# Optimization experiments

Measured on AMD Instinct MI355X. Metric: run time of the kernel, lower is better.

## Reference

```python
import jax, jax.numpy as jnp
import numpy as np
from jax.scipy.linalg import expm

N, D, COND_DIM = 1152, 64, 1152
B, T = 16, 1024


def setup_inputs() -> dict:
    key = jax.random.key(0)
    k1, k2, k3, k4, k5 = jax.random.split(key, 5)
    x = jax.random.normal(k1, (B, T, N), dtype=jnp.float32)
    cond = jax.random.normal(k2, (B, COND_DIM), dtype=jnp.float32)
    # learned parameters
    P = jax.random.normal(k3, (N, D), dtype=jnp.float32)
    n_skew = D * (D - 1) // 2
    # nn.Linear default init: U(-1/sqrt(fan_in), 1/sqrt(fan_in))
    bound = 1.0 / np.sqrt(COND_DIM)
    W = jax.random.uniform(k4, (n_skew, COND_DIM), minval=-bound, maxval=bound, dtype=jnp.float32)
    b = jax.random.uniform(k5, (n_skew,), minval=-bound, maxval=bound, dtype=jnp.float32)
    return {"x": x, "cond": cond, "P": P, "W": W, "b": b}


def _rotation(cond, W, b):
    # SiLU -> Linear -> skew-symmetric A -> matrix exponential
    v = jax.nn.silu(cond) @ W.T + b  # (B, D*(D-1)//2)
    iu, ju = jnp.triu_indices(D, k=1)
    A = jnp.zeros((cond.shape[0], D, D), dtype=v.dtype)
    A = A.at[:, iu, ju].set(v).at[:, ju, iu].set(-v)
    return expm(A)  # batched over leading dim, (B, D, D)


def reference(x, cond, P, W, b):
    U, _ = jnp.linalg.qr(P)          # (N, D) orthonormal basis of subspace
    R = _rotation(cond, W, b)        # (B, D, D)
    z = jnp.einsum('btn,nd->btd', x, U)          # project into subspace
    z_rot = jnp.einsum('btd,bde->bte', z, R)     # rotate within subspace
    x_rot = x + jnp.einsum('btd,nd->btn', z_rot - z, U)  # (z_rot - z) @ U.T
    return x_rot
```

## Files before the change

### kernel.cpp

```cpp
#include <hip/hip_runtime.h>
#include <math.h>

#define NN 1152
#define DD 64
#define NSK 2016
#define NB 16
#define NROWS (NB*1024)
#define GPARTS 6
#define KPARTS 6
#define VNBLK 32
#define VBLKS (VNBLK*KPARTS)
#define TOFF (VBLKS + GPARTS)
#define TBLKS 18

typedef short bf16x8 __attribute__((ext_vector_type(8)));
typedef short bf16x4 __attribute__((ext_vector_type(4)));
typedef float f32x4  __attribute__((ext_vector_type(4)));

__device__ __forceinline__ short bfr(float f){
  unsigned u = __float_as_uint(f);
  u += 0x7fffu + ((u >> 16) & 1u);
  return (short)(u >> 16);
}
__device__ __forceinline__ float htof(short h){
  return __uint_as_float(((unsigned)(unsigned short)h) << 16);
}

__global__ __launch_bounds__(256) void k_pre(const float* __restrict__ cond, const float* __restrict__ W,
                                             float* __restrict__ vpart,
                                             const float* __restrict__ P, float* __restrict__ Gpart,
                                             short* __restrict__ Pbf, short* __restrict__ Ptbf){
  __shared__ float Ps[64*68];
  const int tid = threadIdx.x;
  if (blockIdx.x < VBLKS){
    const int nb = blockIdx.x / KPARTS;
    const int kp = blockIdx.x % KPARTS;
    const int lane = tid & 63, wid = tid >> 6;
    const int m = lane & 15, quad = lane >> 4;
    const int n0 = nb*64 + wid*16;
    if (n0 >= NSK) return;
    f32x4 acc = {0.f,0.f,0.f,0.f};
    const float* crow = &cond[m*NN + kp*192 + quad*8];
    const float* wrow = &W[(n0 + m)*NN + kp*192 + quad*8];
    #pragma unroll
    for (int c = 0; c < 6; ++c){
      const float4 ca = *(const float4*)(crow + c*32);
      const float4 cb = *(const float4*)(crow + c*32 + 4);
      const float4 wa = *(const float4*)(wrow + c*32);
      const float4 wb = *(const float4*)(wrow + c*32 + 4);
      bf16x8 a, b;
      const float cv[8] = {ca.x,ca.y,ca.z,ca.w,cb.x,cb.y,cb.z,cb.w};
      const float wv[8] = {wa.x,wa.y,wa.z,wa.w,wb.x,wb.y,wb.z,wb.w};
      #pragma unroll
      for (int j = 0; j < 8; ++j){
        const float xv = cv[j];
        a[j] = bfr(xv / (1.f + __expf(-xv)));
        b[j] = bfr(wv[j]);
      }
      acc = __builtin_amdgcn_mfma_f32_16x16x32_bf16(a, b, acc, 0, 0, 0);
    }
    #pragma unroll
    for (int r = 0; r < 4; ++r)
      vpart[(kp*16 + quad*4 + r)*NSK + n0 + m] = acc[r];
  } else if (blockIdx.x < TOFF){
    const int p = blockIdx.x - VBLKS;
    const int lr = tid >> 4, lc = (tid & 15) * 4;
    const int ti = tid >> 4, tj = tid & 15;
    float acc[4][4];
    #pragma unroll
    for (int i=0;i<4;++i){
      #pragma unroll
      for (int j=0;j<4;++j) acc[i][j]=0.f;
    }
    for (int ch = 0; ch < 3; ++ch){
      const int nn0 = p*192 + ch*64;
      __syncthreads();
      #pragma unroll
      for (int ii = 0; ii < 4; ++ii){
        const float4 pv = *(const float4*)&P[(nn0 + lr + 16*ii)*DD + lc];
        *(float4*)&Ps[(lr + 16*ii)*68 + lc] = pv;
      }
      __syncthreads();
      for (int r = 0; r < 64; ++r){
        const float4 a = *(const float4*)&Ps[r*68 + ti*4];
        const float4 b = *(const float4*)&Ps[r*68 + tj*4];
        const float av[4] = {a.x,a.y,a.z,a.w};
        const float bv[4] = {b.x,b.y,b.z,b.w};
        #pragma unroll
        for (int i=0;i<4;++i){
          #pragma unroll
          for (int j=0;j<4;++j) acc[i][j] = fmaf(av[i], bv[j], acc[i][j]);
        }
      }
    }
    float* g = &Gpart[p*DD*DD];
    #pragma unroll
    for (int i=0;i<4;++i){
      float4 ov = make_float4(acc[i][0], acc[i][1], acc[i][2], acc[i][3]);
      *(float4*)&g[(ti*4+i)*DD + tj*4] = ov;
    }
  } else {
    const int t = blockIdx.x - TOFF;
    const int n0 = t*64;
    for (int idx = tid; idx < 4096; idx += 256)
      Ps[(idx>>6)*68 + (idx&63)] = P[(n0 + (idx>>6))*DD + (idx&63)];
    __syncthreads();
    for (int idx = tid; idx < 4096; idx += 256){
      const int r = idx>>6, c = idx&63;
      Pbf[(n0+r)*DD + c] = bfr(Ps[r*68 + c]);
    }
    for (int idx = tid; idx < 4096; idx += 256){
      const int d = idx>>6, rr = idx&63;
      Ptbf[d*NN + n0 + rr] = bfr(Ps[rr*68 + d]);
    }
  }
}

__device__ __forceinline__ void mmul68(const float* __restrict__ A, const float* __restrict__ B,
                                       float* __restrict__ C, int tid){
  __syncthreads();
  const int w = tid >> 6, lane = tid & 63;
  const int r0 = (w & 3) * 16 + (lane >> 3) * 2;
  const int c0 = (w >> 2) * 32 + (lane & 7) * 4;
  float acc[2][4];
  #pragma unroll
  for (int i=0;i<2;++i){
    #pragma unroll
    for (int j=0;j<4;++j) acc[i][j]=0.f;
  }
  float4 b0 = *(const float4*)&B[0*68 + c0];
  float4 b1 = *(const float4*)&B[1*68 + c0];
  float4 b2 = *(const float4*)&B[2*68 + c0];
  float4 b3 = *(const float4*)&B[3*68 + c0];
  float4 a0 = *(const float4*)&A[(r0    )*68];
  float4 a1 = *(const float4*)&A[(r0 + 1)*68];
  for (int kq = 0; kq < 16; ++kq){
    float4 nb0, nb1, nb2, nb3, na0, na1;
    if (kq < 15){
      const int k4 = (kq+1)*4;
      nb0 = *(const float4*)&B[(k4+0)*68 + c0];
      nb1 = *(const float4*)&B[(k4+1)*68 + c0];
      nb2 = *(const float4*)&B[(k4+2)*68 + c0];
      nb3 = *(const float4*)&B[(k4+3)*68 + c0];
      na0 = *(const float4*)&A[(r0    )*68 + k4];
      na1 = *(const float4*)&A[(r0 + 1)*68 + k4];
    }
    const float av0[4] = {a0.x,a0.y,a0.z,a0.w};
    const float av1[4] = {a1.x,a1.y,a1.z,a1.w};
    const float4 bb[4] = {b0,b1,b2,b3};
    #pragma unroll
    for (int kk=0;kk<4;++kk){
      acc[0][0] = fmaf(av0[kk], bb[kk].x, acc[0][0]);
      acc[0][1] = fmaf(av0[kk], bb[kk].y, acc[0][1]);
      acc[0][2] = fmaf(av0[kk], bb[kk].z, acc[0][2]);
      acc[0][3] = fmaf(av0[kk], bb[kk].w, acc[0][3]);
      acc[1][0] = fmaf(av1[kk], bb[kk].x, acc[1][0]);
      acc[1][1] = fmaf(av1[kk], bb[kk].y, acc[1][1]);
      acc[1][2] = fmaf(av1[kk], bb[kk].z, acc[1][2]);
      acc[1][3] = fmaf(av1[kk], bb[kk].w, acc[1][3]);
    }
    b0 = nb0; b1 = nb1; b2 = nb2; b3 = nb3; a0 = na0; a1 = na1;
  }
  *(float4*)&C[(r0    )*68 + c0] = make_float4(acc[0][0],acc[0][1],acc[0][2],acc[0][3]);
  *(float4*)&C[(r0 + 1)*68 + c0] = make_float4(acc[1][0],acc[1][1],acc[1][2],acc[1][3]);
  __syncthreads();
}

__global__ __launch_bounds__(512,1) void k_fused(const float* __restrict__ Gpart, const float* __restrict__ P,
                                                 const float* __restrict__ vpart, const float* __restrict__ bias,
                                                 float* __restrict__ Mg, float* __restrict__ Rg,
                                                 const float* __restrict__ x, const short* __restrict__ Ptbf,
                                                 short* __restrict__ ybf){
  __shared__ float Bs[64*68], B2[64*68], B3[64*68], Tb[64*68], Xb[64*68];
  __shared__ float red[512];
  __shared__ float scl_s;
  __shared__ int   ssh_s;
  const int tid = threadIdx.x;
  if (blockIdx.x > NB){
    const int lane = tid & 63, wid = tid >> 6;
    const int row0 = (blockIdx.x - NB - 1) * 64;
    const int m    = lane & 15, quad = lane >> 4;
    const int r0 = (wid & 3) * 16;
    const int c0 = (wid >> 2) * 32;
    f32x4 acc0 = {0.f,0.f,0.f,0.f}, acc1 = {0.f,0.f,0.f,0.f};
    const float* xrow = &x[(row0 + r0 + m)*NN + quad*8];
    const short* ut0  = &Ptbf[(c0      + m)*NN + quad*8];
    const short* ut1  = &Ptbf[(c0 + 16 + m)*NN + quad*8];
    float4 xa = *(const float4*)(xrow);
    float4 xb = *(const float4*)(xrow + 4);
    bf16x8 b0 = *(const bf16x8*)(ut0);
    bf16x8 b1 = *(const bf16x8*)(ut1);
    for (int kc = 0; kc < NN; kc += 32){
      float4 nxa, nxb; bf16x8 nb0, nb1;
      if (kc + 32 < NN){
        nxa = *(const float4*)(xrow + kc + 32);
        nxb = *(const float4*)(xrow + kc + 36);
        nb0 = *(const bf16x8*)(ut0 + kc + 32);
        nb1 = *(const bf16x8*)(ut1 + kc + 32);
      }
      bf16x8 a;
      a[0]=bfr(xa.x); a[1]=bfr(xa.y); a[2]=bfr(xa.z); a[3]=bfr(xa.w);
      a[4]=bfr(xb.x); a[5]=bfr(xb.y); a[6]=bfr(xb.z); a[7]=bfr(xb.w);
      acc0 = __builtin_amdgcn_mfma_f32_16x16x32_bf16(a, b0, acc0, 0, 0, 0);
      acc1 = __builtin_amdgcn_mfma_f32_16x16x32_bf16(a, b1, acc1, 0, 0, 0);
      xa = nxa; xb = nxb; b0 = nb0; b1 = nb1;
    }
    #pragma unroll
    for (int q = 0; q < 4; ++q){
      ybf[(row0 + r0 + quad*4 + q)*DD + c0      + m] = bfr(acc0[q]);
      ybf[(row0 + r0 + quad*4 + q)*DD + c0 + 16 + m] = bfr(acc1[q]);
    }
    return;
  }
  if (blockIdx.x == NB){
    if (tid < 64){
      const int j = tid;
      float Gc[DD], Wc[DD], Rc[DD];
      #pragma unroll
      for (int i = 0; i < DD; ++i){
        float g = 0.f;
        #pragma unroll
        for (int p = 0; p < GPARTS; ++p) g += Gpart[p*4096 + i*DD + j];
        Gc[i] = g;
        Wc[i] = P[i*DD + j];
      }
      #pragma unroll
      for (int k = 0; k < DD; ++k){
        const float gkk = __shfl(Gc[k], k);
        const float wkk = __shfl(Wc[k], k);
        const float beta = (wkk >= 0.f) ? -sqrtf(gkk) : sqrtf(gkk);
        const float wkj = Wc[k];
        const float dj  = Gc[k] - beta*wkj;
        const float cj  = dj / (beta*(beta - wkk));
        float rkj = wkj + dj/beta;
        if (j == k) rkj = beta;
        if (j <  k) rkj = 0.f;
        Rc[k] = rkj;
        #pragma unroll
        for (int i = k+1; i < DD; ++i){
          const float wik = __shfl(Wc[i], k);
          const float rki = __shfl(rkj, i);
          Wc[i] = fmaf(-cj,  wik, Wc[i]);
          Gc[i] = fmaf(-rki, rkj, Gc[i]);
        }
      }
      #pragma unroll
      for (int i = 0; i < DD; ++i) Rg[i*DD + j] = Rc[i];
    }
    return;
  }
  const int b = blockIdx.x;
  for (int idx = tid; idx < 64*64; idx += 512)
    Xb[(idx>>6)*68 + (idx&63)] = 0.f;
  __syncthreads();
  for (int idx = tid; idx < NSK; idx += 512){
    int i = (int)((127.0f - sqrtf(16129.0f - 8.0f*(float)idx)) * 0.5f);
    while (i*(127 - i)/2 > idx) --i;
    while ((i+1)*(127 - (i+1))/2 <= idx) ++i;
    const int jj = idx - i*(127 - i)/2 + i + 1;
    float val = bias[idx];
    #pragma unroll
    for (int p = 0; p < KPARTS; ++p) val += vpart[(p*16 + b)*NSK + idx];
    Xb[i*68 + jj] = val;
    Xb[jj*68 + i] = -val;
  }
  __syncthreads();
  {
    const int c = tid & 63, g = tid >> 6;
    float s = 0.f;
    for (int r = g*8; r < g*8 + 8; ++r) s += fabsf(Xb[r*68 + c]);
    red[g*64 + c] = s;
    __syncthreads();
    if (tid < 64){
      float cs = 0.f;
      #pragma unroll
      for (int g2 = 0; g2 < 8; ++g2) cs += red[g2*64 + tid];
      #pragma unroll
      for (int off = 32; off > 0; off >>= 1) cs = fmaxf(cs, __shfl_xor(cs, off));
      if (tid == 0){
        int s2 = 0; float scale = 1.f;
        float nrm = cs;
        while (nrm > 1.0f && s2 < 40){ nrm *= 0.5f; scale *= 0.5f; ++s2; }
        ssh_s = s2; scl_s = scale;
      }
    }
    __syncthreads();
  }
  const float scale = scl_s;
  const int   sq    = ssh_s;
  for (int idx = tid; idx < 64*64; idx += 512){
    const int i = idx>>6, jj = idx&63;
    Bs[i*68 + jj] = Xb[i*68 + jj] * scale;
  }
  mmul68(Bs, Bs, B2, tid);
  mmul68(B2, Bs, B3, tid);
  for (int idx = tid; idx < 64*64; idx += 512){
    const int i = idx>>6, jj = idx&63;
    const int o = i*68 + jj;
    Tb[o] = (i==jj ? (1.f/720.f) : 0.f) + Bs[o]*(1.f/5040.f) + B2[o]*(1.f/40320.f) + B3[o]*(1.f/362880.f);
  }
  mmul68(B3, Tb, Xb, tid);
  for (int idx = tid; idx < 64*64; idx += 512){
    const int i = idx>>6, jj = idx&63;
    const int o = i*68 + jj;
    Xb[o] += (i==jj ? (1.f/6.f) : 0.f) + Bs[o]*(1.f/24.f) + B2[o]*(1.f/120.f);
  }
  mmul68(B3, Xb, Tb, tid);
  for (int idx = tid; idx < 64*64; idx += 512){
    const int i = idx>>6, jj = idx&63;
    const int o = i*68 + jj;
    Tb[o] += (i==jj ? 1.f : 0.f) + Bs[o] + B2[o]*0.5f;
  }
  float* cur = Tb;
  float* oth = Xb;
  for (int r = 0; r < sq; ++r){
    mmul68(cur, cur, oth, tid);
    float* t = cur; cur = oth; oth = t;
  }
  for (int idx = tid; idx < 64*64; idx += 512){
    const int i = idx>>6, jj = idx&63;
    Mg[b*4096 + idx] = cur[i*68 + jj] - (i==jj ? 1.f : 0.f);
  }
}

__global__ __launch_bounds__(256) void k_kmat(const float* __restrict__ Rg, const float* __restrict__ Mg,
                                              float* __restrict__ Kg){
  __shared__ float Ri[64*68], Ms[64*68], Ts[64*68];
  __shared__ float rd[64];
  const int b = blockIdx.x, tid = threadIdx.x;
  float* Rf = Ts;
  for (int idx = tid; idx < 4096; idx += 256){
    Rf[idx] = Rg[idx];
    Ms[(idx>>6)*68 + (idx&63)] = Mg[b*4096 + idx];
  }
  __syncthreads();
  if (tid < 64) rd[tid] = 1.f / Rf[tid*DD + tid];
  __syncthreads();
  if (tid < 64){
    float u[DD];
    #pragma unroll
    for (int j = 0; j < DD; ++j){
      float s0 = (tid == j) ? 1.f : 0.f, s1 = 0.f;
      #pragma unroll
      for (int l = 0; l + 1 < j; l += 2){
        s0 = fmaf(-u[l],   Rf[l*DD + j],     s0);
        s1 = fmaf(-u[l+1], Rf[(l+1)*DD + j], s1);
      }
      if (j & 1) s0 = fmaf(-u[j-1], Rf[(j-1)*DD + j], s0);
      u[j] = (s0 + s1) * rd[j];
    }
    #pragma unroll
    for (int c = 0; c < DD; ++c) Ri[tid*68 + c] = u[c];
  }
  __syncthreads();
  const int ti = tid >> 4, tj = tid & 15;
  {
    float acc[4][4];
    #pragma unroll
    for (int i=0;i<4;++i){
      #pragma unroll
      for (int j=0;j<4;++j) acc[i][j]=0.f;
    }
    for (int kq = 0; kq < 16; ++kq){
      float4 a[4], bm[4];
      #pragma unroll
      for (int i=0;i<4;++i) a[i] = *(const float4*)&Ri[(ti*4+i)*68 + kq*4];
      #pragma unroll
      for (int kk=0;kk<4;++kk) bm[kk] = *(const float4*)&Ms[(kq*4+kk)*68 + tj*4];
      #pragma unroll
      for (int i=0;i<4;++i){
        const float av[4] = {a[i].x,a[i].y,a[i].z,a[i].w};
        #pragma unroll
        for (int kk=0;kk<4;++kk){
          acc[i][0] = fmaf(av[kk], bm[kk].x, acc[i][0]);
          acc[i][1] = fmaf(av[kk], bm[kk].y, acc[i][1]);
          acc[i][2] = fmaf(av[kk], bm[kk].z, acc[i][2]);
          acc[i][3] = fmaf(av[kk], bm[kk].w, acc[i][3]);
        }
      }
    }
    __syncthreads();
    #pragma unroll
    for (int i=0;i<4;++i)
      *(float4*)&Ts[(ti*4+i)*68 + tj*4] = make_float4(acc[i][0],acc[i][1],acc[i][2],acc[i][3]);
    __syncthreads();
  }
  {
    float acc[4][4];
    #pragma unroll
    for (int i=0;i<4;++i){
      #pragma unroll
      for (int j=0;j<4;++j) acc[i][j]=0.f;
    }
    for (int kq = 0; kq < 16; ++kq){
      float4 a[4], bt[4];
      #pragma unroll
      for (int i=0;i<4;++i) a[i] = *(const float4*)&Ts[(ti*4+i)*68 + kq*4];
      #pragma unroll
      for (int j=0;j<4;++j) bt[j] = *(const float4*)&Ri[(tj*4+j)*68 + kq*4];
      #pragma unroll
      for (int i=0;i<4;++i){
        #pragma unroll
        for (int j=0;j<4;++j){
          acc[i][j] = fmaf(a[i].x, bt[j].x, acc[i][j]);
          acc[i][j] = fmaf(a[i].y, bt[j].y, acc[i][j]);
          acc[i][j] = fmaf(a[i].z, bt[j].z, acc[i][j]);
          acc[i][j] = fmaf(a[i].w, bt[j].w, acc[i][j]);
        }
      }
    }
    #pragma unroll
    for (int i=0;i<4;++i)
      *(float4*)&Kg[b*4096 + (ti*4+i)*DD + tj*4] = make_float4(acc[i][0],acc[i][1],acc[i][2],acc[i][3]);
  }
}

__global__ __launch_bounds__(256) void k_wout(const float* __restrict__ x, const short* __restrict__ Pbf,
                                              const short* __restrict__ ybf, const float* __restrict__ Kg,
                                              float* __restrict__ out){
  __shared__ float Ks[64*68];
  __shared__ float ys[16*68];
  __shared__ short wbf[16*72];
  __shared__ float os[2][16*68];
  const int tid  = threadIdx.x;
  const int lane = tid & 63, wid = tid >> 6;
  const int row0 = blockIdx.x * 16;
  const int bb   = row0 >> 10;
  const int m    = lane & 15, quad = lane >> 4;
  for (int idx = tid; idx < 4096; idx += 256)
    Ks[(idx>>6)*68 + (idx&63)] = Kg[bb*4096 + idx];
  {
    const int idx = tid*4;
    const int r = idx >> 6, c = idx & 63;
    bf16x4 yv = *(const bf16x4*)&ybf[(row0 + r)*DD + c];
    ys[r*68 + c    ] = htof(yv[0]);
    ys[r*68 + c + 1] = htof(yv[1]);
    ys[r*68 + c + 2] = htof(yv[2]);
    ys[r*68 + c + 3] = htof(yv[3]);
  }
  __syncthreads();
  {
    const int r = tid >> 4, c4 = (tid & 15)*4;
    float w0[4] = {0.f,0.f,0.f,0.f};
    for (int k = 0; k < 64; ++k){
      const float yr = ys[r*68 + k];
      const float4 kv = *(const float4*)&Ks[k*68 + c4];
      w0[0] = fmaf(yr, kv.x, w0[0]);
      w0[1] = fmaf(yr, kv.y, w0[1]);
      w0[2] = fmaf(yr, kv.z, w0[2]);
      w0[3] = fmaf(yr, kv.w, w0[3]);
    }
    bf16x4 pk;
    #pragma unroll
    for (int jj = 0; jj < 4; ++jj) pk[jj] = bfr(w0[jj]);
    *(bf16x4*)&wbf[r*72 + c4] = pk;
  }
  __syncthreads();
  bf16x8 wa0 = *(const bf16x8*)&wbf[m*72 +      quad*8];
  bf16x8 wa1 = *(const bf16x8*)&wbf[m*72 + 32 + quad*8];
  const int er = tid >> 4;
  const int ec = (tid & 15) * 4;
  for (int it = 0; it < 18; ++it){
    const int n0 = it*64 + wid*16;
    bf16x8 ub0 = *(const bf16x8*)&Pbf[(n0 + m)*DD +      quad*8];
    bf16x8 ub1 = *(const bf16x8*)&Pbf[(n0 + m)*DD + 32 + quad*8];
    f32x4 acc = {0.f,0.f,0.f,0.f};
    acc = __builtin_amdgcn_mfma_f32_16x16x32_bf16(wa0, ub0, acc, 0, 0, 0);
    acc = __builtin_amdgcn_mfma_f32_16x16x32_bf16(wa1, ub1, acc, 0, 0, 0);
    float* ob = os[it & 1];
    #pragma unroll
    for (int q = 0; q < 4; ++q)
      ob[(quad*4 + q)*68 + wid*16 + m] = acc[q];
    __syncthreads();
    const float4 xv = *(const float4*)&x[(row0 + er)*NN + it*64 + ec];
    const float4 ov = *(const float4*)&ob[er*68 + ec];
    *(float4*)&out[(row0 + er)*NN + it*64 + ec] =
        make_float4(xv.x + ov.x, xv.y + ov.y, xv.z + ov.z, xv.w + ov.w);
  }
}

extern "C" void kernel_launch(void* const* d_in, const int* in_sizes, int n_in,
                              void* d_out, int out_size, void* d_ws, size_t ws_size,
                              hipStream_t stream) {
  const float* x    = (const float*)d_in[0];
  const float* cond = (const float*)d_in[1];
  const float* P    = (const float*)d_in[2];
  const float* W    = (const float*)d_in[3];
  const float* bias = (const float*)d_in[4];
  float* out = (float*)d_out;
  float* ws  = (float*)d_ws;

  float* Gpart = ws;
  float* vpart = ws + 24576;
  float* Kg    = ws + 24576;
  float* Mg    = ws + 218112;
  float* Rg    = ws + 283648;
  short* Pbf   = (short*)(ws + 287744);
  short* Ptbf  = (short*)(ws + 324608);
  short* ybf   = (short*)(ws + 361472);

  hipLaunchKernelGGL(k_pre,  dim3(VBLKS + GPARTS + TBLKS), dim3(256), 0, stream,
                     cond, W, vpart, P, Gpart, Pbf, Ptbf);
  hipLaunchKernelGGL(k_fused, dim3(NB + 1 + NROWS/64), dim3(512), 0, stream,
                     Gpart, P, vpart, bias, Mg, Rg, x, Ptbf, ybf);
  hipLaunchKernelGGL(k_kmat, dim3(NB), dim3(256), 0, stream, Rg, Mg, Kg);
  hipLaunchKernelGGL(k_wout, dim3(NROWS/16), dim3(256), 0, stream, x, Pbf, ybf, Kg, out);
}
```

Measured before the change: 237.7 us.

## Precompute per-batch P·Kᵀ in kmat and simplify output kernel to one GEMM

```diff
diff --git a/kernel.cpp b/kernel.cpp
--- a/kernel.cpp
+++ b/kernel.cpp
@@ -324,10 +324,13 @@
 }
 
 __global__ __launch_bounds__(256) void k_kmat(const float* __restrict__ Rg, const float* __restrict__ Mg,
-                                              float* __restrict__ Kg){
+                                              const short* __restrict__ Pbf, short* __restrict__ Qtbf){
   __shared__ float Ri[64*68], Ms[64*68], Ts[64*68];
+  __shared__ short Kbf[64*72];
   __shared__ float rd[64];
   const int b = blockIdx.x, tid = threadIdx.x;
+  const int lane = tid & 63, wid = tid >> 6;
+  const int m = lane & 15, quad = lane >> 4;
   float* Rf = Ts;
   for (int idx = tid; idx < 4096; idx += 256){
     Rf[idx] = Rg[idx];
@@ -411,71 +414,81 @@
     }
     #pragma unroll
     for (int i=0;i<4;++i)
-      *(float4*)&Kg[b*4096 + (ti*4+i)*DD + tj*4] = make_float4(acc[i][0],acc[i][1],acc[i][2],acc[i][3]);
-  }
-}
-
-__global__ __launch_bounds__(256) void k_wout(const float* __restrict__ x, const short* __restrict__ Pbf,
-                                              const short* __restrict__ ybf, const float* __restrict__ Kg,
-                                              float* __restrict__ out){
-  __shared__ float Ks[64*68];
-  __shared__ float ys[16*68];
-  __shared__ short wbf[16*72];
-  __shared__ float os[2][16*68];
+      #pragma unroll
+      for (int j=0;j<4;++j)
+        Kbf[(ti*4+i)*72 + tj*4+j] = bfr(acc[i][j]);
+  }
+  __syncthreads();
+  for (int ch = 0; ch < 18; ++ch){
+    const int n0 = ch*64;
+    const bf16x8 a0 = *(const bf16x8*)&Pbf[(n0 + wid*16 + m)*DD +      quad*8];
+    const bf16x8 a1 = *(const bf16x8*)&Pbf[(n0 + wid*16 + m)*DD + 32 + quad*8];
+    #pragma unroll
+    for (int ct = 0; ct < 4; ++ct){
+      const bf16x8 b0 = *(const bf16x8*)&Kbf[(ct*16 + m)*72 +      quad*8];
+      const bf16x8 b1 = *(const bf16x8*)&Kbf[(ct*16 + m)*72 + 32 + quad*8];
+      f32x4 acc = {0.f,0.f,0.f,0.f};
+      acc = __builtin_amdgcn_mfma_f32_16x16x32_bf16(a0, b0, acc, 0, 0, 0);
+      acc = __builtin_amdgcn_mfma_f32_16x16x32_bf16(a1, b1, acc, 0, 0, 0);
+      #pragma unroll
+      for (int q = 0; q < 4; ++q)
+        Ms[(wid*16 + quad*4 + q)*68 + ct*16 + m] = acc[q];
+    }
+    __syncthreads();
+    {
+      const int r = tid >> 2, c16 = (tid & 3) * 16;
+      bf16x8 p0, p1;
+      #pragma unroll
+      for (int j = 0; j < 8; ++j){
+        p0[j] = bfr(Ms[r*68 + c16 + j]);
+        p1[j] = bfr(Ms[r*68 + c16 + 8 + j]);
+      }
+      *(bf16x8*)&Qtbf[(b*NN + n0 + r)*DD + c16]     = p0;
+      *(bf16x8*)&Qtbf[(b*NN + n0 + r)*DD + c16 + 8] = p1;
+    }
+    __syncthreads();
+  }
+}
+
+__global__ __launch_bounds__(256) void k_out2(const float* __restrict__ x, const short* __restrict__ Qtbf,
+                                              const short* __restrict__ ybf, float* __restrict__ out){
   const int tid  = threadIdx.x;
   const int lane = tid & 63, wid = tid >> 6;
   const int row0 = blockIdx.x * 16;
   const int bb   = row0 >> 10;
   const int m    = lane & 15, quad = lane >> 4;
-  for (int idx = tid; idx < 4096; idx += 256)
-    Ks[(idx>>6)*68 + (idx&63)] = Kg[bb*4096 + idx];
-  {
-    const int idx = tid*4;
-    const int r = idx >> 6, c = idx & 63;
-    bf16x4 yv = *(const bf16x4*)&ybf[(row0 + r)*DD + c];
-    ys[r*68 + c    ] = htof(yv[0]);
-    ys[r*68 + c + 1] = htof(yv[1]);
-    ys[r*68 + c + 2] = htof(yv[2]);
-    ys[r*68 + c + 3] = htof(yv[3]);
-  }
-  __syncthreads();
-  {
-    const int r = tid >> 4, c4 = (tid & 15)*4;
-    float w0[4] = {0.f,0.f,0.f,0.f};
-    for (int k = 0; k < 64; ++k){
-      const float yr = ys[r*68 + k];
-      const float4 kv = *(const float4*)&Ks[k*68 + c4];
-      w0[0] = fmaf(yr, kv.x, w0[0]);
-      w0[1] = fmaf(yr, kv.y, w0[1]);
-      w0[2] = fmaf(yr, kv.z, w0[2]);
-      w0[3] = fmaf(yr, kv.w, w0[3]);
-    }
-    bf16x4 pk;
-    #pragma unroll
-    for (int jj = 0; jj < 4; ++jj) pk[jj] = bfr(w0[jj]);
-    *(bf16x4*)&wbf[r*72 + c4] = pk;
-  }
-  __syncthreads();
-  bf16x8 wa0 = *(const bf16x8*)&wbf[m*72 +      quad*8];
-  bf16x8 wa1 = *(const bf16x8*)&wbf[m*72 + 32 + quad*8];
-  const int er = tid >> 4;
-  const int ec = (tid & 15) * 4;
+  const int q4   = quad * 4;
+  const short* Qb = &Qtbf[bb*NN*DD];
+  bf16x8 ya0 = *(const bf16x8*)&ybf[(row0 + m)*DD +      quad*8];
+  bf16x8 ya1 = *(const bf16x8*)&ybf[(row0 + m)*DD + 32 + quad*8];
+  bf16x8 qb0 = *(const bf16x8*)&Qb[(wid*16 + m)*DD +      quad*8];
+  bf16x8 qb1 = *(const bf16x8*)&Qb[(wid*16 + m)*DD + 32 + quad*8];
+  float xq0 = x[(row0 + q4 + 0)*NN + wid*16 + m];
+  float xq1 = x[(row0 + q4 + 1)*NN + wid*16 + m];
+  float xq2 = x[(row0 + q4 + 2)*NN + wid*16 + m];
+  float xq3 = x[(row0 + q4 + 3)*NN + wid*16 + m];
   for (int it = 0; it < 18; ++it){
-    const int n0 = it*64 + wid*16;
-    bf16x8 ub0 = *(const bf16x8*)&Pbf[(n0 + m)*DD +      quad*8];
-    bf16x8 ub1 = *(const bf16x8*)&Pbf[(n0 + m)*DD + 32 + quad*8];
+    const int n0 = (wid + 4*it) * 16;
     f32x4 acc = {0.f,0.f,0.f,0.f};
-    acc = __builtin_amdgcn_mfma_f32_16x16x32_bf16(wa0, ub0, acc, 0, 0, 0);
-    acc = __builtin_amdgcn_mfma_f32_16x16x32_bf16(wa1, ub1, acc, 0, 0, 0);
-    float* ob = os[it & 1];
-    #pragma unroll
-    for (int q = 0; q < 4; ++q)
-      ob[(quad*4 + q)*68 + wid*16 + m] = acc[q];
-    __syncthreads();
-    const float4 xv = *(const float4*)&x[(row0 + er)*NN + it*64 + ec];
-    const float4 ov = *(const float4*)&ob[er*68 + ec];
-    *(float4*)&out[(row0 + er)*NN + it*64 + ec] =
-        make_float4(xv.x + ov.x, xv.y + ov.y, xv.z + ov.z, xv.w + ov.w);
+    acc = __builtin_amdgcn_mfma_f32_16x16x32_bf16(ya0, qb0, acc, 0, 0, 0);
+    acc = __builtin_amdgcn_mfma_f32_16x16x32_bf16(ya1, qb1, acc, 0, 0, 0);
+    const float o0 = xq0 + acc[0];
+    const float o1 = xq1 + acc[1];
+    const float o2 = xq2 + acc[2];
+    const float o3 = xq3 + acc[3];
+    if (it < 17){
+      const int n1 = n0 + 64;
+      qb0 = *(const bf16x8*)&Qb[(n1 + m)*DD +      quad*8];
+      qb1 = *(const bf16x8*)&Qb[(n1 + m)*DD + 32 + quad*8];
+      xq0 = x[(row0 + q4 + 0)*NN + n1 + m];
+      xq1 = x[(row0 + q4 + 1)*NN + n1 + m];
+      xq2 = x[(row0 + q4 + 2)*NN + n1 + m];
+      xq3 = x[(row0 + q4 + 3)*NN + n1 + m];
+    }
+    out[(row0 + q4 + 0)*NN + n0 + m] = o0;
+    out[(row0 + q4 + 1)*NN + n0 + m] = o1;
+    out[(row0 + q4 + 2)*NN + n0 + m] = o2;
+    out[(row0 + q4 + 3)*NN + n0 + m] = o3;
   }
 }
 
@@ -492,17 +505,17 @@
 
   float* Gpart = ws;
   float* vpart = ws + 24576;
-  float* Kg    = ws + 24576;
   float* Mg    = ws + 218112;
   float* Rg    = ws + 283648;
   short* Pbf   = (short*)(ws + 287744);
   short* Ptbf  = (short*)(ws + 324608);
   short* ybf   = (short*)(ws + 361472);
+  short* Qtbf  = (short*)(ws + 885760);
 
   hipLaunchKernelGGL(k_pre,  dim3(VBLKS + GPARTS + TBLKS), dim3(256), 0, stream,
                      cond, W, vpart, P, Gpart, Pbf, Ptbf);
   hipLaunchKernelGGL(k_fused, dim3(NB + 1 + NROWS/64), dim3(512), 0, stream,
                      Gpart, P, vpart, bias, Mg, Rg, x, Ptbf, ybf);
-  hipLaunchKernelGGL(k_kmat, dim3(NB), dim3(256), 0, stream, Rg, Mg, Kg);
-  hipLaunchKernelGGL(k_wout, dim3(NROWS/16), dim3(256), 0, stream, x, Pbf, ybf, Kg, out);
-}
+  hipLaunchKernelGGL(k_kmat, dim3(NB), dim3(256), 0, stream, Rg, Mg, Pbf, Qtbf);
+  hipLaunchKernelGGL(k_out2, dim3(NROWS/16), dim3(256), 0, stream, x, Qtbf, ybf, out);
+}
```

New measurement: 250.4 us. +5.3%, slower.
